# Performance work log

Hardware: AMD Instinct MI355X
Metric: run time of the kernel (lower is better)

## Reference

```python
import jax, jax.numpy as jnp
import numpy as np

B, S, D, H = 2, 2048, 1024, 16
HD = D // H  # head_dim = 64
SCALE = HD ** -0.5


def setup_inputs() -> dict:
    key = jax.random.key(0)
    ks = jax.random.split(key, 10)
    std = D ** -0.5
    return {
        "x": jax.random.normal(ks[0], (B, S, D), jnp.float32),
        "y": jax.random.normal(ks[1], (B, S, D), jnp.float32),
        "Wq": jax.random.normal(ks[2], (D, D), jnp.float32) * std,
        "bq": jnp.zeros((D,), jnp.float32),
        "Wk": jax.random.normal(ks[3], (D, D), jnp.float32) * std,
        "bk": jnp.zeros((D,), jnp.float32),
        "Wv": jax.random.normal(ks[4], (D, D), jnp.float32) * std,
        "bv": jnp.zeros((D,), jnp.float32),
        "Wo": jax.random.normal(ks[5], (D, D), jnp.float32) * std,
        "bo": jnp.zeros((D,), jnp.float32),
    }


def reference(x, y, Wq, bq, Wk, bk, Wv, bv, Wo, bo):
    # Linear projections (torch Linear: x @ W.T + b; here W stored as [in,out])
    q = x @ Wq + bq  # [B,S,D]
    k = y @ Wk + bk
    v = y @ Wv + bv
    # split heads -> [B,H,S,hd]
    q = q.reshape(B, S, H, HD).transpose(0, 2, 1, 3)
    k = k.reshape(B, S, H, HD).transpose(0, 2, 1, 3)
    v = v.reshape(B, S, H, HD).transpose(0, 2, 1, 3)
    scores = jnp.einsum("bhqd,bhkd->bhqk", q, k) * SCALE  # [B,H,S,S]
    causal = jnp.tril(jnp.ones((S, S), dtype=bool))  # keep lower triangle
    scores = jnp.where(causal[None, None], scores, -jnp.inf)
    attn = jax.nn.softmax(scores, axis=-1)
    out = jnp.einsum("bhqk,bhkd->bhqd", attn, v)  # [B,H,S,hd]
    out = out.transpose(0, 2, 1, 3).reshape(B, S, D)
    return out @ Wo + bo
```

## Files before the change

### kernel.cpp

```cpp
#include <hip/hip_runtime.h>
#include <hip/hip_bf16.h>


#define BDIM 2
#define SDIM 2048
#define DDIM 1024
#define HDIM 16
#define HD   64
#define MDIM (BDIM*SDIM)
#define C2 0.18033688011112042f

using short8  = __attribute__((ext_vector_type(8))) short;
using floatx4 = __attribute__((ext_vector_type(4))) float;

static __device__ __forceinline__ unsigned short f2bf(float x) {
    union { float f; unsigned int u; } c; c.f = x;
    unsigned int r = (c.u + 0x7fffu + ((c.u >> 16) & 1u)) >> 16;
    return (unsigned short)r;
}

static __device__ __forceinline__ unsigned int pack2bf(float a, float b) {
    union { float f; unsigned int u; } ua, ub;
    ua.f = a; ub.f = b;
    return __builtin_amdgcn_perm(ub.u + 0x8000u, ua.u + 0x8000u, 0x07060302u);
}

#define GLD16(g, l) __builtin_amdgcn_global_load_lds(                        \
    (const __attribute__((address_space(1))) void*)(g),                      \
    (__attribute__((address_space(3))) void*)(l), 16, 0, 0)

__global__ __launch_bounds__(256) void cast_bf16_kernel(
    const float* __restrict__ X, const float* __restrict__ Y,
    unsigned short* __restrict__ Xo, unsigned short* __restrict__ Yo)
{
    const float* A    = blockIdx.z ? Y : X;
    unsigned short* O = blockIdx.z ? Yo : Xo;
    const int idx = blockIdx.x * 256 + threadIdx.x;
    const float4 a = ((const float4*)A)[idx*2];
    const float4 b = ((const float4*)A)[idx*2 + 1];
    ushort4 lo, hi;
    lo.x = f2bf(a.x); lo.y = f2bf(a.y); lo.z = f2bf(a.z); lo.w = f2bf(a.w);
    hi.x = f2bf(b.x); hi.y = f2bf(b.y); hi.z = f2bf(b.z); hi.w = f2bf(b.w);
    ((ushort4*)O)[idx*2]     = lo;
    ((ushort4*)O)[idx*2 + 1] = hi;
}

__global__ __launch_bounds__(256) void wtrans_kernel(
    const float* __restrict__ W0, const float* __restrict__ W1,
    const float* __restrict__ W2, const float* __restrict__ W3,
    unsigned short* __restrict__ T0, unsigned short* __restrict__ T1,
    unsigned short* __restrict__ T2, unsigned short* __restrict__ T3)
{
    __shared__ float tile[64][68];
    const int z = blockIdx.z;
    const float* W    = (z == 0) ? W0 : (z == 1) ? W1 : (z == 2) ? W2 : W3;
    unsigned short* T = (z == 0) ? T0 : (z == 1) ? T1 : (z == 2) ? T2 : T3;
    const int k0 = blockIdx.x * 64, n0 = blockIdx.y * 64;
    const int t = threadIdx.x;
    #pragma unroll
    for (int i = 0; i < 4; ++i) {
        const int idx = t + i*256;
        const int kr = idx >> 4, c4 = idx & 15;
        float4 v = *(const float4*)&W[(size_t)(k0 + kr) * DDIM + n0 + c4*4];
        tile[kr][c4*4+0] = v.x; tile[kr][c4*4+1] = v.y;
        tile[kr][c4*4+2] = v.z; tile[kr][c4*4+3] = v.w;
    }
    __syncthreads();
    #pragma unroll
    for (int i = 0; i < 4; ++i) {
        const int idx = t + i*256;
        const int nr = idx >> 4, kc = idx & 15;
        ushort4 o;
        o.x = f2bf(tile[kc*4+0][nr]); o.y = f2bf(tile[kc*4+1][nr]);
        o.z = f2bf(tile[kc*4+2][nr]); o.w = f2bf(tile[kc*4+3][nr]);
        *(ushort4*)&T[(size_t)(n0 + nr) * DDIM + k0 + kc*4] = o;
    }
}

template <bool SWAP>
__device__ __forceinline__ void gemm128_core(
    const unsigned short* __restrict__ A, const unsigned short* __restrict__ Bt,
    int bm, int bn, unsigned short* As, unsigned short* Bs, floatx4 acc[4][4])
{
    const int t = threadIdx.x;
    const int w = t >> 6, l = t & 63;
    const int quad = l >> 4, col = l & 15;
    const int wr = (w >> 1) * 64, wc = (w & 1) * 64;

    const int c1 = t + 256;
    const int r0 = t >> 2,  o0 = (t & 3) * 8;
    const int r1 = c1 >> 2, o1 = (c1 & 3) * 8;

    const unsigned short* Ar0 = A  + (size_t)(bm + r0) * DDIM + o0;
    const unsigned short* Ar1 = A  + (size_t)(bm + r1) * DDIM + o1;
    const unsigned short* Br0 = Bt + (size_t)(bn + r0) * DDIM + o0;
    const unsigned short* Br1 = Bt + (size_t)(bn + r1) * DDIM + o1;

    for (int kt = 0; kt < DDIM; kt += 32) {
        __syncthreads();
        GLD16(Ar0 + kt, As + t*8);
        GLD16(Ar1 + kt, As + c1*8);
        GLD16(Br0 + kt, Bs + t*8);
        GLD16(Br1 + kt, Bs + c1*8);
        __syncthreads();
        short8 af[4], bfr[4];
        #pragma unroll
        for (int i = 0; i < 4; ++i)
            af[i] = *(const short8*)&As[(wr + i*16 + col)*32 + quad*8];
        #pragma unroll
        for (int j = 0; j < 4; ++j)
            bfr[j] = *(const short8*)&Bs[(wc + j*16 + col)*32 + quad*8];
        #pragma unroll
        for (int i = 0; i < 4; ++i)
            #pragma unroll
            for (int j = 0; j < 4; ++j)
                acc[i][j] = SWAP
                    ? __builtin_amdgcn_mfma_f32_16x16x32_bf16(bfr[j], af[i], acc[i][j], 0, 0, 0)
                    : __builtin_amdgcn_mfma_f32_16x16x32_bf16(af[i], bfr[j], acc[i][j], 0, 0, 0);
    }
}

__global__ __launch_bounds__(256) void qkv_gemm_kernel(
    const unsigned short* __restrict__ xbf, const unsigned short* __restrict__ ybf,
    const unsigned short* __restrict__ Wqt, const unsigned short* __restrict__ Wkt,
    const unsigned short* __restrict__ Wvt,
    const float* __restrict__ bq, const float* __restrict__ bk,
    const float* __restrict__ bv,
    unsigned short* __restrict__ Qbf, unsigned short* __restrict__ Kbf,
    unsigned short* __restrict__ vT)
{
    __shared__ __align__(16) unsigned short As[128*32];
    __shared__ __align__(16) unsigned short Bs[128*32];

    const int z = blockIdx.z;
    const unsigned short* A  = (z == 0) ? xbf : ybf;
    const unsigned short* Wt = (z == 0) ? Wqt : (z == 1) ? Wkt : Wvt;
    const float* bp          = (z == 0) ? bq  : (z == 1) ? bk  : bv;

    const int bm = blockIdx.y * 128, bn = blockIdx.x * 128;
    const int t = threadIdx.x;
    const int w = t >> 6, l = t & 63;
    const int quad = l >> 4, col = l & 15;
    const int wr = (w >> 1) * 64, wc = (w & 1) * 64;

    floatx4 acc[4][4] = {};

    if (z < 2) {
        gemm128_core<true>(A, Wt, bm, bn, As, Bs, acc);
        unsigned short* O = (z == 0) ? Qbf : Kbf;
        const float sc = (z == 0) ? C2 : 1.0f;
        float4 bias4[4];
        #pragma unroll
        for (int j = 0; j < 4; ++j)
            bias4[j] = *(const float4*)&bp[bn + wc + j*16 + quad*4];
        #pragma unroll
        for (int i = 0; i < 4; ++i) {
            const int m = bm + wr + i*16 + col;
            unsigned short* rowp = O + (size_t)m * DDIM;
            #pragma unroll
            for (int j = 0; j < 4; ++j) {
                const float v0 = (acc[i][j][0] + bias4[j].x) * sc;
                const float v1 = (acc[i][j][1] + bias4[j].y) * sc;
                const float v2 = (acc[i][j][2] + bias4[j].z) * sc;
                const float v3 = (acc[i][j][3] + bias4[j].w) * sc;
                uint2 pk;
                pk.x = pack2bf(v0, v1);
                pk.y = pack2bf(v2, v3);
                *(uint2*)&rowp[bn + wc + j*16 + quad*4] = pk;
            }
        }
    } else {
        gemm128_core<false>(A, Wt, bm, bn, As, Bs, acc);
        #pragma unroll
        for (int j = 0; j < 4; ++j) {
            const int gn = bn + wc + j*16 + col;
            const float bias = bp[gn];
            #pragma unroll
            for (int i = 0; i < 4; ++i) {
                const int gm0 = bm + wr + i*16 + quad*4;
                uint2 pk;
                pk.x = pack2bf(acc[i][j][0] + bias, acc[i][j][1] + bias);
                pk.y = pack2bf(acc[i][j][2] + bias, acc[i][j][3] + bias);
                *(uint2*)&vT[((size_t)((gm0 >> 11) * DDIM + gn)) * SDIM + (gm0 & 2047)] = pk;
            }
        }
    }
}

__global__ __launch_bounds__(256) void out_gemm_kernel(
    const unsigned short* __restrict__ Obf, const unsigned short* __restrict__ Wot,
    const float* __restrict__ bo, float* __restrict__ out)
{
    __shared__ __align__(16) unsigned short As[128*32];
    __shared__ __align__(16) unsigned short Bs[64*32];

    const int t = threadIdx.x;
    const int w = t >> 6, l = t & 63;
    const int quad = l >> 4, col = l & 15;
    const int bm = blockIdx.y * 128, bn = blockIdx.x * 64;
    const int wr = (w >> 1) * 64, wc = (w & 1) * 32;

    const int r0 = t >> 2, o0 = (t & 3) * 8;
    const unsigned short* Ar0 = Obf + (size_t)(bm + r0) * DDIM + o0;
    const unsigned short* Ar1 = Obf + (size_t)(bm + 64 + r0) * DDIM + o0;
    const unsigned short* Br  = Wot + (size_t)(bn + r0) * DDIM + o0;

    floatx4 acc[4][2] = {};

    for (int kt = 0; kt < DDIM; kt += 32) {
        __syncthreads();
        GLD16(Ar0 + kt, As + t*8);
        GLD16(Ar1 + kt, As + (t + 256)*8);
        GLD16(Br  + kt, Bs + t*8);
        __syncthreads();
        short8 af[4], bfr[2];
        #pragma unroll
        for (int i = 0; i < 4; ++i)
            af[i] = *(const short8*)&As[(wr + i*16 + col)*32 + quad*8];
        #pragma unroll
        for (int j = 0; j < 2; ++j)
            bfr[j] = *(const short8*)&Bs[(wc + j*16 + col)*32 + quad*8];
        #pragma unroll
        for (int i = 0; i < 4; ++i)
            #pragma unroll
            for (int j = 0; j < 2; ++j)
                acc[i][j] = __builtin_amdgcn_mfma_f32_16x16x32_bf16(
                    bfr[j], af[i], acc[i][j], 0, 0, 0);
    }

    float4 bias4[2];
    #pragma unroll
    for (int j = 0; j < 2; ++j)
        bias4[j] = *(const float4*)&bo[bn + wc + j*16 + quad*4];
    #pragma unroll
    for (int i = 0; i < 4; ++i) {
        const int m = bm + wr + i*16 + col;
        float* rowp = out + (size_t)m * DDIM;
        #pragma unroll
        for (int j = 0; j < 2; ++j) {
            float4 o;
            o.x = acc[i][j][0] + bias4[j].x;
            o.y = acc[i][j][1] + bias4[j].y;
            o.z = acc[i][j][2] + bias4[j].z;
            o.w = acc[i][j][3] + bias4[j].w;
            *(float4*)&rowp[bn + wc + j*16 + quad*4] = o;
        }
    }
}

__global__ __launch_bounds__(256) void attn_mfma_kernel(
    const unsigned short* __restrict__ Qbf, const unsigned short* __restrict__ Kbf,
    const unsigned short* __restrict__ vT, unsigned short* __restrict__ Obf)
{
    __shared__ __align__(16) unsigned short KfL[2][512*8];
    __shared__ __align__(16) unsigned short VfL[2][512*8];
    __shared__ __align__(16) unsigned short PfL[8*1024];

    const int t = threadIdx.x;
    const int w = t >> 6, l = t & 63;
    const int quad = l >> 4, col = l & 15;
    const int jt = blockIdx.x;
    const int h  = blockIdx.y, b = blockIdx.z;
    const size_t hoff = (size_t)h * HD;
    const size_t bS = (size_t)b * SDIM;
    const size_t bD = (size_t)b * DDIM;

    const int qt  = (w < 2) ? jt : (31 - jt);
    const int qwb = qt * 64 + (w & 1) * 32;
    const int nk_wave  = qt + 1;
    const int nk_block = 32 - jt;

    const unsigned short* kp[2];
    const unsigned short* vp[2];
    int kdst[2], vdst[2];
    #pragma unroll
    for (int i = 0; i < 2; ++i) {
        const int f = 2*w + i;
        kp[i]   = Kbf + (bS + (f >> 1)*16 + col) * DDIM + hoff + (f & 1)*32 + quad*8;
        vp[i]   = vT  + (bD + hoff + (f >> 1)*16 + col) * SDIM + (f & 1)*32 + quad*8;
        kdst[i] = (f*64 + l)*8;
        vdst[i] = (f*64 + l)*8;
    }

    short8 qf[2][2];
    #pragma unroll
    for (int qs = 0; qs < 2; ++qs)
        #pragma unroll
        for (int kc = 0; kc < 2; ++kc)
            qf[qs][kc] = *(const short8*)
                &Qbf[(bS + qwb + qs*16 + col) * DDIM + hoff + kc*32 + quad*8];

    float lrun[2] = {0.0f, 0.0f};
    floatx4 o[2][4] = {};

    #pragma unroll
    for (int i = 0; i < 2; ++i) {
        GLD16(kp[i], &KfL[0][kdst[i]]);
        GLD16(vp[i], &VfL[0][vdst[i]]);
    }

    #pragma unroll 1
    for (int it = 0; it < nk_block; ++it) {
        const int ktb = it * 64;
        const int cur = it & 1;
        __syncthreads();
        if (it + 1 < nk_block) {
            const int nxt = cur ^ 1;
            const size_t ko = (size_t)(it + 1) * 64 * DDIM;
            const int    vo = (it + 1) * 64;
            #pragma unroll
            for (int i = 0; i < 2; ++i) {
                GLD16(kp[i] + ko, &KfL[nxt][kdst[i]]);
                GLD16(vp[i] + vo, &VfL[nxt][vdst[i]]);
            }
        }
        if (it >= nk_wave) continue;

        const unsigned short* Kb = KfL[cur];
        const unsigned short* Vb = VfL[cur];
        short8 kf[4][2], vfr[4][2];
        #pragma unroll
        for (int kt = 0; kt < 4; ++kt)
            #pragma unroll
            for (int kc = 0; kc < 2; ++kc)
                kf[kt][kc] = *(const short8*)&Kb[((kt*2 + kc)*64 + l)*8];
        #pragma unroll
        for (int n = 0; n < 4; ++n)
            #pragma unroll
            for (int kk = 0; kk < 2; ++kk)
                vfr[n][kk] = *(const short8*)&Vb[((n*2 + kk)*64 + l)*8];

        #pragma unroll
        for (int qs = 0; qs < 2; ++qs) {
            if (ktb > qwb + qs*16 + 15) continue;

            floatx4 sT[4];
            #pragma unroll
            for (int kt = 0; kt < 4; ++kt) {
                floatx4 z = {};
                z = __builtin_amdgcn_mfma_f32_16x16x32_bf16(kf[kt][0], qf[qs][0], z, 0, 0, 0);
                z = __builtin_amdgcn_mfma_f32_16x16x32_bf16(kf[kt][1], qf[qs][1], z, 0, 0, 0);
                sT[kt] = z;
            }

            const int qrow = qwb + qs*16 + col;
            const bool anymask = (ktb + 63 > qwb + qs*16);
            float p[4][4];
            #pragma unroll
            for (int kt = 0; kt < 4; ++kt)
                #pragma unroll
                for (int r = 0; r < 4; ++r) {
                    float xv = sT[kt][r];
                    if (anymask && (ktb + kt*16 + quad*4 + r > qrow))
                        xv = -1e30f;
                    p[kt][r] = exp2f(xv);
                }

            float st[4];
            #pragma unroll
            for (int kt = 0; kt < 4; ++kt)
                st[kt] = (p[kt][0] + p[kt][1]) + (p[kt][2] + p[kt][3]);
            lrun[qs] += (st[0] + st[1]) + (st[2] + st[3]);

            const int pb = (w*2 + qs) * 1024;
            #pragma unroll
            for (int kt = 0; kt < 4; ++kt) {
                uint2 pk;
                pk.x = pack2bf(p[kt][0], p[kt][1]);
                pk.y = pack2bf(p[kt][2], p[kt][3]);
                *(uint2*)&PfL[pb + ((kt*2 + (quad>>1))*16 + col)*8 + (quad&1)*4] = pk;
            }
            const short8 pf0 = *(const short8*)&PfL[pb + ((0*4 + quad)*16 + col)*8];
            const short8 pf1 = *(const short8*)&PfL[pb + ((1*4 + quad)*16 + col)*8];
            #pragma unroll
            for (int n = 0; n < 4; ++n) {
                o[qs][n] = __builtin_amdgcn_mfma_f32_16x16x32_bf16(vfr[n][0], pf0, o[qs][n], 0, 0, 0);
                o[qs][n] = __builtin_amdgcn_mfma_f32_16x16x32_bf16(vfr[n][1], pf1, o[qs][n], 0, 0, 0);
            }
        }
    }

    #pragma unroll
    for (int qs = 0; qs < 2; ++qs) {
        float lt = lrun[qs];
        lt += __shfl_xor(lt, 16);
        lt += __shfl_xor(lt, 32);
        const float inv = 1.0f / lt;
        #pragma unroll
        for (int n = 0; n < 4; ++n) {
            ushort4 pk;
            pk.x = f2bf(o[qs][n][0] * inv); pk.y = f2bf(o[qs][n][1] * inv);
            pk.z = f2bf(o[qs][n][2] * inv); pk.w = f2bf(o[qs][n][3] * inv);
            *(ushort4*)&Obf[(bS + qwb + qs*16 + col) * DDIM + hoff + n*16 + quad*4] = pk;
        }
    }
}

extern "C" void kernel_launch(void* const* d_in, const int* in_sizes, int n_in,
                              void* d_out, int out_size, void* d_ws, size_t ws_size,
                              hipStream_t stream) {
    const float* x  = (const float*)d_in[0];
    const float* y  = (const float*)d_in[1];
    const float* Wq = (const float*)d_in[2];
    const float* bq = (const float*)d_in[3];
    const float* Wk = (const float*)d_in[4];
    const float* bk = (const float*)d_in[5];
    const float* Wv = (const float*)d_in[6];
    const float* bv = (const float*)d_in[7];
    const float* Wo = (const float*)d_in[8];
    const float* bo = (const float*)d_in[9];
    float* out = (float*)d_out;

    const size_t mat  = (size_t)MDIM * DDIM;
    const size_t wmat = (size_t)DDIM * DDIM;
    unsigned short* p = (unsigned short*)d_ws;
    unsigned short* xbf = p;            p += mat;
    unsigned short* ybf = p;            p += mat;
    unsigned short* Wqt = p;            p += wmat;
    unsigned short* Wkt = p;            p += wmat;
    unsigned short* Wvt = p;            p += wmat;
    unsigned short* Wot = p;            p += wmat;
    unsigned short* Qbf = p;            p += mat;
    unsigned short* Kbf = p;            p += mat;
    unsigned short* vT  = p;            p += mat;
    unsigned short* Obf = p;            p += mat;

    hipLaunchKernelGGL(cast_bf16_kernel, dim3(MDIM*DDIM/8/256, 1, 2), dim3(256),
                       0, stream, x, y, xbf, ybf);
    hipLaunchKernelGGL(wtrans_kernel, dim3(16, 16, 4), dim3(256), 0, stream,
                       Wq, Wk, Wv, Wo, Wqt, Wkt, Wvt, Wot);

    hipLaunchKernelGGL(qkv_gemm_kernel, dim3(DDIM/128, MDIM/128, 3), dim3(256),
                       0, stream, xbf, ybf, Wqt, Wkt, Wvt, bq, bk, bv,
                       Qbf, Kbf, vT);

    hipLaunchKernelGGL(attn_mfma_kernel, dim3(16, HDIM, BDIM), dim3(256),
                       0, stream, Qbf, Kbf, vT, Obf);

    hipLaunchKernelGGL(out_gemm_kernel, dim3(DDIM/64, MDIM/128), dim3(256),
                       0, stream, Obf, Wot, bo, out);
}
```

Measured before the change: 244.6 us.

## Double-buffer GEMM LDS tiles, merge prep kernels, and remap attention tiles

Merges the input cast and weight transpose into one prep kernel launch. Both GEMM kernels get a second LDS buffer so the next K-slice loads while the current one is computed, which also removes one barrier per iteration. The attention kernel changes from pairing a short and a long query tile per block to 128-row query tiles per block, reversing the tile order for the second batch to balance load. These changes trade extra shared memory, which may lower occupancy, and a coarser attention work split for fewer launches and less stalling on loads.

```diff
diff --git a/kernel.cpp b/kernel.cpp
--- a/kernel.cpp
+++ b/kernel.cpp
@@ -29,34 +29,35 @@
     (const __attribute__((address_space(1))) void*)(g),                      \
     (__attribute__((address_space(3))) void*)(l), 16, 0, 0)
 
-__global__ __launch_bounds__(256) void cast_bf16_kernel(
+__global__ __launch_bounds__(256) void prep_kernel(
     const float* __restrict__ X, const float* __restrict__ Y,
-    unsigned short* __restrict__ Xo, unsigned short* __restrict__ Yo)
-{
-    const float* A    = blockIdx.z ? Y : X;
-    unsigned short* O = blockIdx.z ? Yo : Xo;
-    const int idx = blockIdx.x * 256 + threadIdx.x;
-    const float4 a = ((const float4*)A)[idx*2];
-    const float4 b = ((const float4*)A)[idx*2 + 1];
-    ushort4 lo, hi;
-    lo.x = f2bf(a.x); lo.y = f2bf(a.y); lo.z = f2bf(a.z); lo.w = f2bf(a.w);
-    hi.x = f2bf(b.x); hi.y = f2bf(b.y); hi.z = f2bf(b.z); hi.w = f2bf(b.w);
-    ((ushort4*)O)[idx*2]     = lo;
-    ((ushort4*)O)[idx*2 + 1] = hi;
-}
-
-__global__ __launch_bounds__(256) void wtrans_kernel(
     const float* __restrict__ W0, const float* __restrict__ W1,
     const float* __restrict__ W2, const float* __restrict__ W3,
+    unsigned short* __restrict__ Xo, unsigned short* __restrict__ Yo,
     unsigned short* __restrict__ T0, unsigned short* __restrict__ T1,
     unsigned short* __restrict__ T2, unsigned short* __restrict__ T3)
 {
     __shared__ float tile[64][68];
     const int z = blockIdx.z;
-    const float* W    = (z == 0) ? W0 : (z == 1) ? W1 : (z == 2) ? W2 : W3;
-    unsigned short* T = (z == 0) ? T0 : (z == 1) ? T1 : (z == 2) ? T2 : T3;
-    const int k0 = blockIdx.x * 64, n0 = blockIdx.y * 64;
     const int t = threadIdx.x;
+    if (z < 2) {
+        const float* A    = z ? Y : X;
+        unsigned short* O = z ? Yo : Xo;
+        const int idx = blockIdx.x * 256 + t;
+        const float4 a = ((const float4*)A)[idx*2];
+        const float4 b = ((const float4*)A)[idx*2 + 1];
+        ushort4 lo, hi;
+        lo.x = f2bf(a.x); lo.y = f2bf(a.y); lo.z = f2bf(a.z); lo.w = f2bf(a.w);
+        hi.x = f2bf(b.x); hi.y = f2bf(b.y); hi.z = f2bf(b.z); hi.w = f2bf(b.w);
+        ((ushort4*)O)[idx*2]     = lo;
+        ((ushort4*)O)[idx*2 + 1] = hi;
+        return;
+    }
+    if (blockIdx.x >= 256) return;
+    const int zz = z - 2;
+    const float* W    = (zz == 0) ? W0 : (zz == 1) ? W1 : (zz == 2) ? W2 : W3;
+    unsigned short* T = (zz == 0) ? T0 : (zz == 1) ? T1 : (zz == 2) ? T2 : T3;
+    const int k0 = (blockIdx.x & 15) * 64, n0 = (blockIdx.x >> 4) * 64;
     #pragma unroll
     for (int i = 0; i < 4; ++i) {
         const int idx = t + i*256;
@@ -96,20 +97,31 @@
     const unsigned short* Br0 = Bt + (size_t)(bn + r0) * DDIM + o0;
     const unsigned short* Br1 = Bt + (size_t)(bn + r1) * DDIM + o1;
 
+    GLD16(Ar0, As + t*8);
+    GLD16(Ar1, As + c1*8);
+    GLD16(Br0, Bs + t*8);
+    GLD16(Br1, Bs + c1*8);
+
     for (int kt = 0; kt < DDIM; kt += 32) {
+        const int cur = (kt >> 5) & 1;
+        unsigned short* Asn = As + (cur ^ 1) * 4096;
+        unsigned short* Bsn = Bs + (cur ^ 1) * 4096;
         __syncthreads();
-        GLD16(Ar0 + kt, As + t*8);
-        GLD16(Ar1 + kt, As + c1*8);
-        GLD16(Br0 + kt, Bs + t*8);
-        GLD16(Br1 + kt, Bs + c1*8);
-        __syncthreads();
+        if (kt + 32 < DDIM) {
+            GLD16(Ar0 + kt + 32, Asn + t*8);
+            GLD16(Ar1 + kt + 32, Asn + c1*8);
+            GLD16(Br0 + kt + 32, Bsn + t*8);
+            GLD16(Br1 + kt + 32, Bsn + c1*8);
+        }
+        const unsigned short* Asc = As + cur*4096;
+        const unsigned short* Bsc = Bs + cur*4096;
         short8 af[4], bfr[4];
         #pragma unroll
         for (int i = 0; i < 4; ++i)
-            af[i] = *(const short8*)&As[(wr + i*16 + col)*32 + quad*8];
+            af[i] = *(const short8*)&Asc[(wr + i*16 + col)*32 + quad*8];
         #pragma unroll
         for (int j = 0; j < 4; ++j)
-            bfr[j] = *(const short8*)&Bs[(wc + j*16 + col)*32 + quad*8];
+            bfr[j] = *(const short8*)&Bsc[(wc + j*16 + col)*32 + quad*8];
         #pragma unroll
         for (int i = 0; i < 4; ++i)
             #pragma unroll
@@ -129,8 +141,8 @@
     unsigned short* __restrict__ Qbf, unsigned short* __restrict__ Kbf,
     unsigned short* __restrict__ vT)
 {
-    __shared__ __align__(16) unsigned short As[128*32];
-    __shared__ __align__(16) unsigned short Bs[128*32];
+    __shared__ __align__(16) unsigned short As[2*4096];
+    __shared__ __align__(16) unsigned short Bs[2*4096];
 
     const int z = blockIdx.z;
     const unsigned short* A  = (z == 0) ? xbf : ybf;
@@ -191,8 +203,8 @@
     const unsigned short* __restrict__ Obf, const unsigned short* __restrict__ Wot,
     const float* __restrict__ bo, float* __restrict__ out)
 {
-    __shared__ __align__(16) unsigned short As[128*32];
-    __shared__ __align__(16) unsigned short Bs[64*32];
+    __shared__ __align__(16) unsigned short As[2*4096];
+    __shared__ __align__(16) unsigned short Bs[2*2048];
 
     const int t = threadIdx.x;
     const int w = t >> 6, l = t & 63;
@@ -207,19 +219,29 @@
 
     floatx4 acc[4][2] = {};
 
+    GLD16(Ar0, As + t*8);
+    GLD16(Ar1, As + (t + 256)*8);
+    GLD16(Br,  Bs + t*8);
+
     for (int kt = 0; kt < DDIM; kt += 32) {
+        const int cur = (kt >> 5) & 1;
+        unsigned short* Asn = As + (cur ^ 1) * 4096;
+        unsigned short* Bsn = Bs + (cur ^ 1) * 2048;
         __syncthreads();
-        GLD16(Ar0 + kt, As + t*8);
-        GLD16(Ar1 + kt, As + (t + 256)*8);
-        GLD16(Br  + kt, Bs + t*8);
-        __syncthreads();
+        if (kt + 32 < DDIM) {
+            GLD16(Ar0 + kt + 32, Asn + t*8);
+            GLD16(Ar1 + kt + 32, Asn + (t + 256)*8);
+            GLD16(Br  + kt + 32, Bsn + t*8);
+        }
+        const unsigned short* Asc = As + cur*4096;
+        const unsigned short* Bsc = Bs + cur*2048;
         short8 af[4], bfr[2];
         #pragma unroll
         for (int i = 0; i < 4; ++i)
-            af[i] = *(const short8*)&As[(wr + i*16 + col)*32 + quad*8];
+            af[i] = *(const short8*)&Asc[(wr + i*16 + col)*32 + quad*8];
         #pragma unroll
         for (int j = 0; j < 2; ++j)
-            bfr[j] = *(const short8*)&Bs[(wc + j*16 + col)*32 + quad*8];
+            bfr[j] = *(const short8*)&Bsc[(wc + j*16 + col)*32 + quad*8];
         #pragma unroll
         for (int i = 0; i < 4; ++i)
             #pragma unroll
@@ -259,16 +281,14 @@
     const int t = threadIdx.x;
     const int w = t >> 6, l = t & 63;
     const int quad = l >> 4, col = l & 15;
-    const int jt = blockIdx.x;
     const int h  = blockIdx.y, b = blockIdx.z;
+    const int qt = b ? (15 - blockIdx.x) : blockIdx.x;
     const size_t hoff = (size_t)h * HD;
     const size_t bS = (size_t)b * SDIM;
     const size_t bD = (size_t)b * DDIM;
 
-    const int qt  = (w < 2) ? jt : (31 - jt);
-    const int qwb = qt * 64 + (w & 1) * 32;
-    const int nk_wave  = qt + 1;
-    const int nk_block = 32 - jt;
+    const int qwb = qt * 128 + w * 32;
+    const int nk_block = 2*qt + 2;
 
     const unsigned short* kp[2];
     const unsigned short* vp[2];
@@ -314,7 +334,7 @@
                 GLD16(vp[i] + vo, &VfL[nxt][vdst[i]]);
             }
         }
-        if (it >= nk_wave) continue;
+        if (ktb > qwb + 31) continue;
 
         const unsigned short* Kb = KfL[cur];
         const unsigned short* Vb = VfL[cur];
@@ -425,10 +445,9 @@
     unsigned short* vT  = p;            p += mat;
     unsigned short* Obf = p;            p += mat;
 
-    hipLaunchKernelGGL(cast_bf16_kernel, dim3(MDIM*DDIM/8/256, 1, 2), dim3(256),
-                       0, stream, x, y, xbf, ybf);
-    hipLaunchKernelGGL(wtrans_kernel, dim3(16, 16, 4), dim3(256), 0, stream,
-                       Wq, Wk, Wv, Wo, Wqt, Wkt, Wvt, Wot);
+    hipLaunchKernelGGL(prep_kernel, dim3(MDIM*DDIM/8/256, 1, 6), dim3(256),
+                       0, stream, x, y, Wq, Wk, Wv, Wo,
+                       xbf, ybf, Wqt, Wkt, Wvt, Wot);
 
     hipLaunchKernelGGL(qkv_gemm_kernel, dim3(DDIM/128, MDIM/128, 3), dim3(256),
                        0, stream, xbf, ybf, Wqt, Wkt, Wvt, bq, bk, bv,
```

Measured after the change: 238.1 us. -2.7%, faster.
